# Performance work log

Hardware: AMD Instinct MI355X
Metric: run time of the kernel (lower is better)

## Reference

```python
import jax, jax.numpy as jnp
import numpy as np

EMB = 1024
HEADS = 16
HEAD_SIZE = EMB // HEADS


def setup_inputs() -> dict:
    key = jax.random.key(0)
    ks = jax.random.split(key, 10)
    s = 1.0 / np.sqrt(EMB)
    return {
        "x": jax.random.normal(ks[0], (2, 2048, EMB), dtype=jnp.float32),
        "ln_gamma": jnp.ones((EMB,), jnp.float32),
        "ln_beta": jnp.zeros((EMB,), jnp.float32),
        "Wq": jax.random.normal(ks[1], (EMB, EMB), jnp.float32) * s,
        "bq": jnp.zeros((EMB,), jnp.float32),
        "Wk": jax.random.normal(ks[2], (EMB, EMB), jnp.float32) * s,
        "bk": jnp.zeros((EMB,), jnp.float32),
        "Wv": jax.random.normal(ks[3], (EMB, EMB), jnp.float32) * s,
        "bv": jnp.zeros((EMB,), jnp.float32),
        "Wo": jax.random.normal(ks[4], (EMB, EMB), jnp.float32) * s,
        "bo": jnpps if False else jnp.zeros((EMB,), jnp.float32),
    }


def _layernorm(x, gamma, beta, eps=1e-5):
    mu = jnp.mean(x, axis=-1, keepdims=True)
    var = jnp.mean(jnp.square(x - mu), axis=-1, keepdims=True)
    return (x - mu) * jax.lax.rsqrt(var + eps) * gamma + beta


def reference(x, ln_gamma, ln_beta, Wq, bq, Wk, bk, Wv, bv, Wo, bo):
    B, L, D = x.shape
    h = _layernorm(x, ln_gamma, ln_beta)
    # projections -> [B, H, L, hd]
    def split_heads(t):
        return t.reshape(B, L, HEADS, HEAD_SIZE).transpose(0, 2, 1, 3)
    q = split_heads(h @ Wq.T + bq)
    k = split_heads(h @ Wk.T + bk)
    v = split_heads(h @ Wv.T + bv)
    scale = HEAD_SIZE ** (-0.5)
    w = jnp.einsum("bhqd,bhkd->bhqk", q, k) * scale  # [B,H,L,L]
    w = jax.nn.softmax(w, axis=-1)
    o = jnp.einsum("bhqk,bhkd->bhqd", w, v)
    o = o.transpose(0, 2, 1, 3).reshape(B, L, D)
    o = o @ Wo.T + bo
    return x + o
```

## Files before the change

kernel.cpp:

```cpp
#include <hip/hip_runtime.h>
#include <math.h>

#define B_   2
#define L_   2048
#define EMB_ 1024
#define H_   16
#define HD_  64
#define M_   (B_ * L_)
#define KSPLIT 2
#define LOG2E 1.44269504088896f

typedef __bf16 bf16x8 __attribute__((ext_vector_type(8)));
typedef __bf16 bf16x4 __attribute__((ext_vector_type(4)));
typedef __bf16 bf16x2 __attribute__((ext_vector_type(2)));
typedef float floatx16 __attribute__((ext_vector_type(16)));
typedef unsigned int uintx2 __attribute__((ext_vector_type(2)));

typedef __attribute__((address_space(1))) const void GV;
typedef __attribute__((address_space(3))) void LV;

#define MFMA32(a, b, c) __builtin_amdgcn_mfma_f32_32x32x16_bf16((a), (b), (c), 0, 0, 0)

#if __has_builtin(__builtin_amdgcn_exp2f)
#define EXP2(x) __builtin_amdgcn_exp2f(x)
#else
#define EXP2(x) exp2f(x)
#endif

#define SWZ(row) ((((row) & 7) ^ (((row) >> 3) & 3)))

__device__ __forceinline__ int pkbf(float a, float b) {
#if __has_builtin(__builtin_amdgcn_cvt_pk_bf16_f32)
    union { bf16x2 v; int i; } u;
    u.v = __builtin_amdgcn_cvt_pk_bf16_f32(a, b);
    return u.i;
#else
    union { __bf16 h[2]; int i; } u;
    u.h[0] = (__bf16)a; u.h[1] = (__bf16)b;
    return u.i;
#endif
}

__global__ __launch_bounds__(256) void prep_kernel(
        const float* __restrict__ x, const float* __restrict__ gamma,
        const float* __restrict__ beta, __bf16* __restrict__ h,
        const float* __restrict__ s0, const float* __restrict__ s1,
        const float* __restrict__ s2, const float* __restrict__ s3,
        __bf16* __restrict__ d0, __bf16* __restrict__ d1,
        __bf16* __restrict__ d2, __bf16* __restrict__ d3) {
    int bid = blockIdx.x;
    int tid = threadIdx.x;
    if (bid >= M_) {
        int wb = bid - M_;
        int z = wb >> 8;
        const float* s = (z == 0) ? s0 : (z == 1) ? s1 : (z == 2) ? s2 : s3;
        __bf16* d = (z == 0) ? d0 : (z == 1) ? d1 : (z == 2) ? d2 : d3;
        size_t base = (size_t)((wb & 255) * 256 + tid) * 16;
#pragma unroll
        for (int j = 0; j < 4; ++j) {
            float4 f = *(const float4*)(s + base + j * 4);
            bf16x4 t;
            t[0] = (__bf16)f.x; t[1] = (__bf16)f.y; t[2] = (__bf16)f.z; t[3] = (__bf16)f.w;
            *(bf16x4*)(d + base + j * 4) = t;
        }
        return;
    }
    int row = bid;
    const float* xr = x + (size_t)row * EMB_;
    float4 v = *(const float4*)(xr + tid * 4);
    float s  = v.x + v.y + v.z + v.w;
    float ss = v.x * v.x + v.y * v.y + v.z * v.z + v.w * v.w;
    for (int off = 32; off; off >>= 1) {
        s  += __shfl_down(s, off, 64);
        ss += __shfl_down(ss, off, 64);
    }
    __shared__ float s1_[4], s2_[4];
    int wid = tid >> 6;
    if ((tid & 63) == 0) { s1_[wid] = s; s2_[wid] = ss; }
    __syncthreads();
    if (tid == 0) {
        float a = s1_[0] + s1_[1] + s1_[2] + s1_[3];
        float b = s2_[0] + s2_[1] + s2_[2] + s2_[3];
        float mu = a / EMB_;
        float var = b / EMB_ - mu * mu;
        s1_[0] = mu;
        s2_[0] = rsqrtf(var + 1e-5f);
    }
    __syncthreads();
    float mu = s1_[0], rstd = s2_[0];
    float4 g4 = *(const float4*)(gamma + tid * 4);
    float4 b4 = *(const float4*)(beta + tid * 4);
    bf16x4 o;
    o[0] = (__bf16)((v.x - mu) * rstd * g4.x + b4.x);
    o[1] = (__bf16)((v.y - mu) * rstd * g4.y + b4.y);
    o[2] = (__bf16)((v.z - mu) * rstd * g4.z + b4.z);
    o[3] = (__bf16)((v.w - mu) * rstd * g4.w + b4.w);
    *(bf16x4*)(h + (size_t)row * EMB_ + tid * 4) = o;
}

__device__ __forceinline__ void stage_tile128(const __bf16* gbase, __bf16* lds,
                                              int wave, int lane) {
    int srow = lane >> 3;
    int gch0 = lane & 7;
#pragma unroll
    for (int s = 0; s < 4; ++s) {
        int seg = wave * 4 + s;
        int row = seg * 8 + srow;
        int g = gch0 ^ SWZ(row);
        __builtin_amdgcn_global_load_lds(
            (GV*)(gbase + (size_t)row * EMB_ + g * 8),
            (LV*)(lds + seg * 512 + lane * 8), 16, 0, 0);
    }
}

__global__ __launch_bounds__(256) void gemm_qkv_mfma(
        const __bf16* __restrict__ A, const __bf16* __restrict__ W,
        const float* __restrict__ bq, const float* __restrict__ bk,
        const float* __restrict__ bv,
        __bf16* __restrict__ Qo, __bf16* __restrict__ Ko,
        __bf16* __restrict__ Vto) {
    __shared__ __bf16 As[128 * 64];
    __shared__ __bf16 Bs[128 * 64];
    int tid = threadIdx.x, wave = tid >> 6, lane = tid & 63;
    int wm = wave >> 1, wn = wave & 1;
    int quad = lane >> 5, lq = lane & 31;
    int flat = blockIdx.y * gridDim.x + blockIdx.x;
    int nf = (flat & 7) * 96 + (flat >> 3);
    int bm = (nf / 24) * 128, bn = (nf % 24) * 128;

    floatx16 acc[2][2];
#pragma unroll
    for (int i = 0; i < 2; ++i)
#pragma unroll
        for (int j = 0; j < 2; ++j)
#pragma unroll
            for (int r = 0; r < 16; ++r) acc[i][j][r] = 0.f;

    for (int k0 = 0; k0 < EMB_; k0 += 64) {
        __syncthreads();
        stage_tile128(A + (size_t)bm * EMB_ + k0, As, wave, lane);
        stage_tile128(W + (size_t)bn * EMB_ + k0, Bs, wave, lane);
        __syncthreads();
#pragma unroll
        for (int s = 0; s < 4; ++s) {
            int g = 2 * s + quad;
            int r0 = wm * 64 + lq, r1 = r0 + 32;
            int c0 = wn * 64 + lq, c1 = c0 + 32;
            bf16x8 a0 = *(const bf16x8*)&As[r0 * 64 + ((g ^ SWZ(r0)) * 8)];
            bf16x8 a1 = *(const bf16x8*)&As[r1 * 64 + ((g ^ SWZ(r1)) * 8)];
            bf16x8 b0 = *(const bf16x8*)&Bs[c0 * 64 + ((g ^ SWZ(c0)) * 8)];
            bf16x8 b1 = *(const bf16x8*)&Bs[c1 * 64 + ((g ^ SWZ(c1)) * 8)];
            acc[0][0] = MFMA32(a0, b0, acc[0][0]);
            acc[0][1] = MFMA32(a0, b1, acc[0][1]);
            acc[1][0] = MFMA32(a1, b0, acc[1][0]);
            acc[1][1] = MFMA32(a1, b1, acc[1][1]);
        }
    }

#pragma unroll
    for (int mb = 0; mb < 2; ++mb) {
#pragma unroll
        for (int nb = 0; nb < 2; ++nb) {
            int col = bn + wn * 64 + nb * 32 + lq;
            int z = col >> 10;
            int cc = col & 1023;
            float bv_ = (z == 0) ? bq[cc] : (z == 1) ? bk[cc] : bv[cc];
            if (z < 2) {
                __bf16* dst = (z == 0) ? Qo : Ko;
                float qs = (z == 0) ? 0.125f * LOG2E : 1.0f;
#pragma unroll
                for (int r = 0; r < 16; ++r) {
                    int row = bm + wm * 64 + mb * 32 + (r & 3) + 8 * (r >> 2) + 4 * quad;
                    dst[(size_t)row * EMB_ + cc] = (__bf16)((acc[mb][nb][r] + bv_) * qs);
                }
            } else {
                int hh = cc >> 6, d = cc & 63;
#pragma unroll
                for (int rb = 0; rb < 4; ++rb) {
                    int row = bm + wm * 64 + mb * 32 + 8 * rb + 4 * quad;
                    int b = row >> 11, l = row & (L_ - 1);
                    bf16x4 t;
#pragma unroll
                    for (int a = 0; a < 4; ++a) t[a] = (__bf16)(acc[mb][nb][4 * rb + a] + bv_);
                    *(bf16x4*)(Vto + ((size_t)(b * H_ + hh) * HD_ + d) * L_ + l) = t;
                }
            }
        }
    }
}

__global__ __launch_bounds__(256) void gemm_out_mfma(
        const __bf16* __restrict__ A, const __bf16* __restrict__ W,
        const float* __restrict__ bias, const float* __restrict__ x,
        float* __restrict__ out) {
    __shared__ __bf16 As[128 * 64];
    __shared__ __bf16 Bs[128 * 64];
    int tid = threadIdx.x, wave = tid >> 6, lane = tid & 63;
    int wm = wave >> 1, wn = wave & 1;
    int quad = lane >> 5, lq = lane & 31;
    int flat = blockIdx.y * gridDim.x + blockIdx.x;
    int nf = (flat & 7) * 32 + (flat >> 3);
    int bm = (nf / 8) * 128, bn = (nf % 8) * 128;

    floatx16 acc[2][2];
#pragma unroll
    for (int i = 0; i < 2; ++i)
#pragma unroll
        for (int j = 0; j < 2; ++j)
#pragma unroll
            for (int r = 0; r < 16; ++r) acc[i][j][r] = 0.f;

    for (int k0 = 0; k0 < EMB_; k0 += 64) {
        __syncthreads();
        stage_tile128(A + (size_t)bm * EMB_ + k0, As, wave, lane);
        stage_tile128(W + (size_t)bn * EMB_ + k0, Bs, wave, lane);
        __syncthreads();
#pragma unroll
        for (int s = 0; s < 4; ++s) {
            int g = 2 * s + quad;
            int r0 = wm * 64 + lq, r1 = r0 + 32;
            int c0 = wn * 64 + lq, c1 = c0 + 32;
            bf16x8 a0 = *(const bf16x8*)&As[r0 * 64 + ((g ^ SWZ(r0)) * 8)];
            bf16x8 a1 = *(const bf16x8*)&As[r1 * 64 + ((g ^ SWZ(r1)) * 8)];
            bf16x8 b0 = *(const bf16x8*)&Bs[c0 * 64 + ((g ^ SWZ(c0)) * 8)];
            bf16x8 b1 = *(const bf16x8*)&Bs[c1 * 64 + ((g ^ SWZ(c1)) * 8)];
            acc[0][0] = MFMA32(a0, b0, acc[0][0]);
            acc[0][1] = MFMA32(a0, b1, acc[0][1]);
            acc[1][0] = MFMA32(a1, b0, acc[1][0]);
            acc[1][1] = MFMA32(a1, b1, acc[1][1]);
        }
    }

#pragma unroll
    for (int mb = 0; mb < 2; ++mb) {
#pragma unroll
        for (int nb = 0; nb < 2; ++nb) {
            int col = bn + wn * 64 + nb * 32 + lq;
            float bv_ = bias[col];
#pragma unroll
            for (int r = 0; r < 16; ++r) {
                size_t row = bm + wm * 64 + mb * 32 + (r & 3) + 8 * (r >> 2) + 4 * quad;
                out[row * EMB_ + col] = acc[mb][nb][r] + bv_ + x[row * EMB_ + col];
            }
        }
    }
}

__global__ __launch_bounds__(512, 2) void attn_mfma(
        const __bf16* __restrict__ Q,
        const __bf16* __restrict__ K,
        const __bf16* __restrict__ Vt,
        __bf16* __restrict__ Op,
        float* __restrict__ Lp,
        __bf16* __restrict__ Ob,
        int ks, int fin) {
    __shared__ __bf16 smem[18432];
    __bf16* KsB = smem;
    __bf16* VsB = smem + 8192;
    __bf16* Tsm = smem;

    int tid = threadIdx.x, wave = tid >> 6, lane = tid & 63;
    int quad = lane >> 5, lq = lane & 31;
    int bh = blockIdx.x;
    int b = bh >> 4, h = bh & 15;
    int q0 = blockIdx.y * 256 + wave * 32;
    const size_t tok0 = (size_t)b * L_;

    const __bf16* Kb = K + tok0 * EMB_ + h * HD_;
    const __bf16* Vb = Vt + (size_t)bh * HD_ * L_;

    bf16x8 qf[4];
    {
        const __bf16* qp = Q + (tok0 + q0 + lq) * EMB_ + h * HD_ + quad * 8;
#pragma unroll
        for (int s = 0; s < 4; ++s) qf[s] = *(const bf16x8*)(qp + s * 16);
    }

    floatx16 oacc[2];
#pragma unroll
    for (int j = 0; j < 2; ++j)
#pragma unroll
        for (int r = 0; r < 16; ++r) oacc[j][r] = 0.f;
    float lacc = 0.f;

    int srow = lane >> 3, gch0 = lane & 7;

    auto stage = [&](int buf, int kt) {
        int row = wave * 8 + srow;
        int g = gch0 ^ SWZ(row);
        __builtin_amdgcn_global_load_lds(
            (GV*)(Kb + (size_t)(kt + row) * EMB_ + g * 8),
            (LV*)(KsB + buf * 4096 + wave * 512 + lane * 8), 16, 0, 0);
        __builtin_amdgcn_global_load_lds(
            (GV*)(Vb + (size_t)row * L_ + kt + g * 8),
            (LV*)(VsB + buf * 4096 + wave * 512 + lane * 8), 16, 0, 0);
    };

    auto compute = [&](int buf) {
#pragma unroll
        for (int nb = 0; nb < 2; ++nb) {
            int krow = nb * 32 + lq;
            bf16x8 kf[4];
#pragma unroll
            for (int s = 0; s < 4; ++s)
                kf[s] = *(const bf16x8*)(KsB + buf * 4096 + krow * 64 + (((2 * s + quad) ^ SWZ(krow)) * 8));

            floatx16 sacc;
#pragma unroll
            for (int r = 0; r < 16; ++r) sacc[r] = 0.f;
            __builtin_amdgcn_s_setprio(1);
#pragma unroll
            for (int s = 0; s < 4; ++s) sacc = MFMA32(kf[s], qf[s], sacc);
            __builtin_amdgcn_s_setprio(0);

            int P[8];
            float lsum = 0.f;
#pragma unroll
            for (int t = 0; t < 8; ++t) {
                float pa = EXP2(sacc[2 * t]);
                float pb = EXP2(sacc[2 * t + 1]);
                lsum += pa + pb;
                P[t] = pkbf(pa, pb);
            }
            lacc += lsum;
            union { int i[4]; bf16x8 v; } bf0, bf1;
#if __has_builtin(__builtin_amdgcn_permlane32_swap)
            {
                uintx2 r;
                r = __builtin_amdgcn_permlane32_swap((unsigned)P[0], (unsigned)P[2], false, false);
                bf0.i[0] = (int)r[0]; bf0.i[2] = (int)r[1];
                r = __builtin_amdgcn_permlane32_swap((unsigned)P[1], (unsigned)P[3], false, false);
                bf0.i[1] = (int)r[0]; bf0.i[3] = (int)r[1];
                r = __builtin_amdgcn_permlane32_swap((unsigned)P[4], (unsigned)P[6], false, false);
                bf1.i[0] = (int)r[0]; bf1.i[2] = (int)r[1];
                r = __builtin_amdgcn_permlane32_swap((unsigned)P[5], (unsigned)P[7], false, false);
                bf1.i[1] = (int)r[0]; bf1.i[3] = (int)r[1];
            }
#else
            int X[8];
#pragma unroll
            for (int t = 0; t < 8; ++t) X[t] = __shfl_xor(P[t], 32, 64);
            bf0.i[0] = quad ? X[2] : P[0];
            bf0.i[1] = quad ? X[3] : P[1];
            bf0.i[2] = quad ? P[2] : X[0];
            bf0.i[3] = quad ? P[3] : X[1];
            bf1.i[0] = quad ? X[6] : P[4];
            bf1.i[1] = quad ? X[7] : P[5];
            bf1.i[2] = quad ? P[6] : X[4];
            bf1.i[3] = quad ? P[7] : X[5];
#endif

            __builtin_amdgcn_s_setprio(1);
#pragma unroll
            for (int half = 0; half < 2; ++half) {
                int t = 2 * nb + half;
#pragma unroll
                for (int db = 0; db < 2; ++db) {
                    int drow = db * 32 + lq;
                    bf16x8 vf = *(const bf16x8*)(VsB + buf * 4096 + drow * 64 + (((2 * t + quad) ^ SWZ(drow)) * 8));
                    oacc[db] = MFMA32(vf, half ? bf1.v : bf0.v, oacc[db]);
                }
            }
            __builtin_amdgcn_s_setprio(0);
        }
    };

    const int kt0 = ks * (L_ / KSPLIT);
    const int NT = (L_ / KSPLIT) / 64;

    stage(0, kt0);
    for (int t = 0; t < NT; ++t) {
        __syncthreads();
        if (t + 1 < NT) stage((t + 1) & 1, kt0 + (t + 1) * 64);
        compute(t & 1);
    }

    float l = lacc + __shfl_xor(lacc, 32, 64);
    if (!fin) {
        if (lane < 32)
            Lp[(size_t)bh * L_ + q0 + lane] = l;
#pragma unroll
        for (int db = 0; db < 2; ++db)
#pragma unroll
            for (int r = 0; r < 16; ++r) {
                int dp = db * 32 + (r & 3) + 8 * (r >> 2) + 4 * quad;
                Op[((size_t)bh * HD_ + dp) * L_ + q0 + lq] = (__bf16)oacc[db][r];
            }
    } else {
        l += Lp[(size_t)bh * L_ + q0 + lq];
        float rl = 1.0f / l;
        __syncthreads();
        int qloc = wave * 32 + lq;
#pragma unroll
        for (int db = 0; db < 2; ++db)
#pragma unroll
            for (int r = 0; r < 16; ++r) {
                int dp = db * 32 + (r & 3) + 8 * (r >> 2) + 4 * quad;
                float p0 = (float)Op[((size_t)bh * HD_ + dp) * L_ + q0 + lq];
                Tsm[qloc * 72 + dp] = (__bf16)((oacc[db][r] + p0) * rl);
            }
        __syncthreads();
        int qblk = blockIdx.y * 256;
#pragma unroll
        for (int cc = 0; cc < 4; ++cc) {
            int tl = cc * 64 + (tid >> 3), dc = (tid & 7) * 8;
            bf16x8 v = *(const bf16x8*)&Tsm[tl * 72 + dc];
            *(bf16x8*)(Ob + ((size_t)b * L_ + qblk + tl) * EMB_ + h * HD_ + dc) = v;
        }
    }
}

extern "C" void kernel_launch(void* const* d_in, const int* in_sizes, int n_in,
                              void* d_out, int out_size, void* d_ws, size_t ws_size,
                              hipStream_t stream) {
    const float* x     = (const float*)d_in[0];
    const float* gamma = (const float*)d_in[1];
    const float* beta  = (const float*)d_in[2];
    const float* Wq    = (const float*)d_in[3];
    const float* bq    = (const float*)d_in[4];
    const float* Wk    = (const float*)d_in[5];
    const float* bk    = (const float*)d_in[6];
    const float* Wv    = (const float*)d_in[7];
    const float* bv    = (const float*)d_in[8];
    const float* Wo    = (const float*)d_in[9];
    const float* bo    = (const float*)d_in[10];
    float* out = (float*)d_out;

    const size_t SLAB = (size_t)M_ * EMB_;
    const size_t WSLAB = (size_t)EMB_ * EMB_;
    char* ws = (char*)d_ws;
    __bf16* hb    = (__bf16*)ws;                      ws += SLAB * 2;
    __bf16* Qb    = (__bf16*)ws;                      ws += SLAB * 2;
    __bf16* Kb    = (__bf16*)ws;                      ws += SLAB * 2;
    __bf16* Vtb   = (__bf16*)ws;                      ws += SLAB * 2;
    __bf16* Wqkvb = (__bf16*)ws;                      ws += 3 * WSLAB * 2;
    __bf16* Wob   = (__bf16*)ws;                      ws += WSLAB * 2;
    __bf16* Op    = (__bf16*)ws;                      ws += (size_t)KSPLIT * SLAB * 2;
    float*  Lp    = (float*)ws;                       ws += (size_t)KSPLIT * 32 * L_ * 4;
    __bf16* Ob    = hb;

    prep_kernel<<<M_ + 1024, 256, 0, stream>>>(
        x, gamma, beta, hb,
        Wq, Wk, Wv, Wo, Wqkvb, Wqkvb + WSLAB, Wqkvb + 2 * WSLAB, Wob);
    gemm_qkv_mfma<<<dim3(3 * EMB_ / 128, M_ / 128), 256, 0, stream>>>(
        hb, Wqkvb, bq, bk, bv, Qb, Kb, Vtb);
    attn_mfma<<<dim3(B_ * H_, L_ / 256), 512, 0, stream>>>(
        Qb, Kb, Vtb, Op, Lp, Ob, 0, 0);
    attn_mfma<<<dim3(B_ * H_, L_ / 256), 512, 0, stream>>>(
        Qb, Kb, Vtb, Op, Lp, Ob, 1, 1);
    gemm_out_mfma<<<dim3(EMB_ / 128, M_ / 128), 256, 0, stream>>>(
        Ob, Wob, bo, x, out);
}
```

Before: 193.1 us.

## Merge split-K attention launches into one grid with atomic last-block combine

Runs both key-range halves of attention in a single launch using a third grid dimension, so 512 blocks run concurrently instead of two serialized 256-block launches. Each block writes its partial output and row sums, and an atomic counter picks the second finisher to merge both halves and write the normalized result. This removes a launch boundary and the serialization between halves, at the cost of extra partial-result traffic for every block plus threadfence and atomic overhead. The counter is reset in the prep kernel.

```diff
diff --git a/kernel.cpp b/kernel.cpp
--- a/kernel.cpp
+++ b/kernel.cpp
@@ -47,9 +47,11 @@
         const float* __restrict__ s0, const float* __restrict__ s1,
         const float* __restrict__ s2, const float* __restrict__ s3,
         __bf16* __restrict__ d0, __bf16* __restrict__ d1,
-        __bf16* __restrict__ d2, __bf16* __restrict__ d3) {
+        __bf16* __restrict__ d2, __bf16* __restrict__ d3,
+        unsigned* __restrict__ done) {
     int bid = blockIdx.x;
     int tid = threadIdx.x;
+    if (bid == 0) done[tid] = 0u;
     if (bid >= M_) {
         int wb = bid - M_;
         int z = wb >> 8;
@@ -253,15 +255,17 @@
         __bf16* __restrict__ Op,
         float* __restrict__ Lp,
         __bf16* __restrict__ Ob,
-        int ks, int fin) {
+        unsigned* __restrict__ done) {
     __shared__ __bf16 smem[18432];
     __bf16* KsB = smem;
     __bf16* VsB = smem + 8192;
     __bf16* Tsm = smem;
+    __shared__ int winner;
 
     int tid = threadIdx.x, wave = tid >> 6, lane = tid & 63;
     int quad = lane >> 5, lq = lane & 31;
     int bh = blockIdx.x;
+    int ks = blockIdx.z;
     int b = bh >> 4, h = bh & 15;
     int q0 = blockIdx.y * 256 + wave * 32;
     const size_t tok0 = (size_t)b * L_;
@@ -376,37 +380,47 @@
     }
 
     float l = lacc + __shfl_xor(lacc, 32, 64);
-    if (!fin) {
-        if (lane < 32)
-            Lp[(size_t)bh * L_ + q0 + lane] = l;
-#pragma unroll
-        for (int db = 0; db < 2; ++db)
-#pragma unroll
-            for (int r = 0; r < 16; ++r) {
-                int dp = db * 32 + (r & 3) + 8 * (r >> 2) + 4 * quad;
-                Op[((size_t)bh * HD_ + dp) * L_ + q0 + lq] = (__bf16)oacc[db][r];
-            }
-    } else {
-        l += Lp[(size_t)bh * L_ + q0 + lq];
-        float rl = 1.0f / l;
-        __syncthreads();
-        int qloc = wave * 32 + lq;
-#pragma unroll
-        for (int db = 0; db < 2; ++db)
-#pragma unroll
-            for (int r = 0; r < 16; ++r) {
-                int dp = db * 32 + (r & 3) + 8 * (r >> 2) + 4 * quad;
-                float p0 = (float)Op[((size_t)bh * HD_ + dp) * L_ + q0 + lq];
-                Tsm[qloc * 72 + dp] = (__bf16)((oacc[db][r] + p0) * rl);
-            }
-        __syncthreads();
-        int qblk = blockIdx.y * 256;
-#pragma unroll
-        for (int cc = 0; cc < 4; ++cc) {
-            int tl = cc * 64 + (tid >> 3), dc = (tid & 7) * 8;
-            bf16x8 v = *(const bf16x8*)&Tsm[tl * 72 + dc];
-            *(bf16x8*)(Ob + ((size_t)b * L_ + qblk + tl) * EMB_ + h * HD_ + dc) = v;
-        }
+
+    if (lane < 32)
+        Lp[((size_t)ks * 32 + bh) * L_ + q0 + lane] = l;
+#pragma unroll
+    for (int db = 0; db < 2; ++db)
+#pragma unroll
+        for (int r = 0; r < 16; ++r) {
+            int dp = db * 32 + (r & 3) + 8 * (r >> 2) + 4 * quad;
+            Op[((size_t)(ks * 32 + bh) * HD_ + dp) * L_ + q0 + lq] =
+                (__bf16)oacc[db][r];
+        }
+
+    __threadfence();
+    __syncthreads();
+    if (tid == 0) {
+        unsigned old = atomicAdd(&done[bh * 8 + blockIdx.y], 1u);
+        winner = (old == 1u);
+    }
+    __syncthreads();
+    if (!winner) return;
+    __threadfence();
+
+    int other = 1 - ks;
+    float lo = Lp[((size_t)other * 32 + bh) * L_ + q0 + lq];
+    float rl = 1.0f / (l + lo);
+    int qloc = wave * 32 + lq;
+#pragma unroll
+    for (int db = 0; db < 2; ++db)
+#pragma unroll
+        for (int r = 0; r < 16; ++r) {
+            int dp = db * 32 + (r & 3) + 8 * (r >> 2) + 4 * quad;
+            float p0 = (float)Op[((size_t)(other * 32 + bh) * HD_ + dp) * L_ + q0 + lq];
+            Tsm[qloc * 72 + dp] = (__bf16)((oacc[db][r] + p0) * rl);
+        }
+    __syncthreads();
+    int qblk = blockIdx.y * 256;
+#pragma unroll
+    for (int cc = 0; cc < 4; ++cc) {
+        int tl = cc * 64 + (tid >> 3), dc = (tid & 7) * 8;
+        bf16x8 v = *(const bf16x8*)&Tsm[tl * 72 + dc];
+        *(bf16x8*)(Ob + ((size_t)b * L_ + qblk + tl) * EMB_ + h * HD_ + dc) = v;
     }
 }
 
@@ -437,17 +451,16 @@
     __bf16* Wob   = (__bf16*)ws;                      ws += WSLAB * 2;
     __bf16* Op    = (__bf16*)ws;                      ws += (size_t)KSPLIT * SLAB * 2;
     float*  Lp    = (float*)ws;                       ws += (size_t)KSPLIT * 32 * L_ * 4;
+    unsigned* done = (unsigned*)ws;                   ws += 256 * 4;
     __bf16* Ob    = hb;
 
     prep_kernel<<<M_ + 1024, 256, 0, stream>>>(
         x, gamma, beta, hb,
-        Wq, Wk, Wv, Wo, Wqkvb, Wqkvb + WSLAB, Wqkvb + 2 * WSLAB, Wob);
+        Wq, Wk, Wv, Wo, Wqkvb, Wqkvb + WSLAB, Wqkvb + 2 * WSLAB, Wob, done);
     gemm_qkv_mfma<<<dim3(3 * EMB_ / 128, M_ / 128), 256, 0, stream>>>(
         hb, Wqkvb, bq, bk, bv, Qb, Kb, Vtb);
-    attn_mfma<<<dim3(B_ * H_, L_ / 256), 512, 0, stream>>>(
-        Qb, Kb, Vtb, Op, Lp, Ob, 0, 0);
-    attn_mfma<<<dim3(B_ * H_, L_ / 256), 512, 0, stream>>>(
-        Qb, Kb, Vtb, Op, Lp, Ob, 1, 1);
+    attn_mfma<<<dim3(B_ * H_, L_ / 256, KSPLIT), 512, 0, stream>>>(
+        Qb, Kb, Vtb, Op, Lp, Ob, done);
     gemm_out_mfma<<<dim3(EMB_ / 128, M_ / 128), 256, 0, stream>>>(
         Ob, Wob, bo, x, out);
 }
```

New measurement: 352.4 us. 1.83x slower.
